# Optimization experiments

Hardware: AMD Instinct MI355X
Metric: run time of the kernel (lower is better)

## Reference

```python
import jax, jax.numpy as jnp
import numpy as np

N, IN_DIM, OUT_DIM, HEADS = 4096, 128, 32, 4
EDGE_PROB = 0.015  # ~61 neighbors/node on average


def setup_inputs() -> dict:
    key = jax.random.key(0)
    k1, k2, k3, k4 = jax.random.split(key, 4)
    x = jax.random.normal(k1, (N, IN_DIM), dtype=jnp.float32)
    adj = (jax.random.uniform(k2, (N, N)) < EDGE_PROB).astype(jnp.float32)
    adj = jnp.maximum(adj, jnp.eye(N, dtype=jnp.float32))  # self loops so softmax is never all-masked
    # nn.Linear(in_dim, out_dim*heads, bias=False): weight stored here as [in, out]
    W = jax.random.normal(k3, (IN_DIM, OUT_DIM * HEADS), dtype=jnp.float32) / np.sqrt(IN_DIM).astype(np.float32)
    # nn.Linear(2*out_dim, 1, bias=False) -> a single [2*out_dim] vector shared across heads
    a = jax.random.normal(k4, (2 * OUT_DIM,), dtype=jnp.float32) / np.sqrt(2 * OUT_DIM).astype(np.float32)
    return {"x": x, "adj": adj, "W": W, "a": a}


def reference(x, adj, W, a):
    n = x.shape[0]
    xp = (x @ W).reshape(n, HEADS, OUT_DIM)  # [N, H, D]
    # Original builds concat([x_expanded, x_j_expanded])[i,j] = [x[j] || x[i]] and applies
    # a linear map. Since attn is linear, scores decompose: e[i,j,h] = a1.x[j,h] + a2.x[i,h].
    a_j, a_i = a[:OUT_DIM], a[OUT_DIM:]
    s_j = jnp.einsum('nhd,d->nh', xp, a_j)  # contribution of column node j
    s_i = jnp.einsum('nhd,d->nh', xp, a_i)  # contribution of row node i
    scale = jnp.float32(1.0 / np.sqrt(OUT_DIM))
    e = (s_i[:, None, :] + s_j[None, :, :]) * scale  # [N, N, H]
    e = e + ((1.0 - adj) * jnp.float32(-1e9))[:, :, None]
    att = jax.nn.softmax(e, axis=1)  # softmax over dim=1 (neighbors j), as in original
    out = jnp.einsum('ijh,jhd->ihd', att, xp)  # attention-weighted neighbor aggregation
    return out.reshape(n, HEADS * OUT_DIM)
```

## Files before the change

### kernel.cpp

```cpp
#include <hip/hip_runtime.h>

#define N_NODES 4096
#define IN_DIM  128
#define OUT_DIM 32
#define HEADS   4
#define FDIM    128
#define K1_ROWS 8
#define CAP     192

static __device__ __forceinline__ unsigned bf16pack(float a, float b) {
    unsigned ua = __float_as_uint(a), ub = __float_as_uint(b);
    ua = (ua + 0x7FFFu + ((ua >> 16) & 1u)) >> 16;
    ub = (ub + 0x7FFFu + ((ub >> 16) & 1u)) >> 16;
    return ua | (ub << 16);
}

__global__ __launch_bounds__(256) void gat_proj(const float* __restrict__ x,
                                                const float* __restrict__ W,
                                                const float* __restrict__ a,
                                                unsigned* __restrict__ Ybf,
                                                float* __restrict__ Eg) {
    __shared__ float xs[K1_ROWS * IN_DIM];
    __shared__ float eS[K1_ROWS][HEADS];
    const int t    = threadIdx.x;
    const int row0 = blockIdx.x * K1_ROWS;

    ((float4*)xs)[t] = ((const float4*)(x + (size_t)row0 * IN_DIM))[t];
    __syncthreads();

    const int c  = t & 127;
    const int rg = t >> 7;
    const float* xb = xs + (rg * 4) * IN_DIM;

    float acc0 = 0.f, acc1 = 0.f, acc2 = 0.f, acc3 = 0.f;
#pragma unroll 4
    for (int k0 = 0; k0 < IN_DIM; k0 += 4) {
        const float w0 = W[(k0 + 0) * FDIM + c];
        const float w1 = W[(k0 + 1) * FDIM + c];
        const float w2 = W[(k0 + 2) * FDIM + c];
        const float w3 = W[(k0 + 3) * FDIM + c];
        const float4 x0 = *(const float4*)(xb + 0 * IN_DIM + k0);
        const float4 x1 = *(const float4*)(xb + 1 * IN_DIM + k0);
        const float4 x2 = *(const float4*)(xb + 2 * IN_DIM + k0);
        const float4 x3 = *(const float4*)(xb + 3 * IN_DIM + k0);
        acc0 = fmaf(x0.x, w0, fmaf(x0.y, w1, fmaf(x0.z, w2, fmaf(x0.w, w3, acc0))));
        acc1 = fmaf(x1.x, w0, fmaf(x1.y, w1, fmaf(x1.z, w2, fmaf(x1.w, w3, acc1))));
        acc2 = fmaf(x2.x, w0, fmaf(x2.y, w1, fmaf(x2.z, w2, fmaf(x2.w, w3, acc2))));
        acc3 = fmaf(x3.x, w0, fmaf(x3.y, w1, fmaf(x3.z, w2, fmaf(x3.w, w3, acc3))));
    }

    const int rb = rg * 4;
    __syncthreads();
    xs[(rb + 0) * FDIM + c] = acc0;
    xs[(rb + 1) * FDIM + c] = acc1;
    xs[(rb + 2) * FDIM + c] = acc2;
    xs[(rb + 3) * FDIM + c] = acc3;
    __syncthreads();

    if (t < K1_ROWS * HEADS) {
        const int r = t >> 2, h = t & 3;
        const float4* xr = (const float4*)(xs + r * FDIM + h * OUT_DIM);
        const float4* aj = (const float4*)a;
        float vj = 0.f;
#pragma unroll
        for (int q = 0; q < 8; ++q) {
            const float4 xv = xr[q], a0 = aj[q];
            vj += xv.x * a0.x + xv.y * a0.y + xv.z * a0.z + xv.w * a0.w;
        }
        const float e = __expf(vj * 0.17677669529663687f);
        eS[r][h] = e;
        Eg[(row0 + r) * HEADS + h] = e;
    }
    __syncthreads();

#pragma unroll
    for (int q = 0; q < 2; ++q) {
        const int idx = t + 256 * q;
        const int r   = idx >> 6;
        const int cp  = idx & 63;
        const float e = eS[r][cp >> 4];
        const float a0 = xs[r * FDIM + 2 * cp]     * e;
        const float a1 = xs[r * FDIM + 2 * cp + 1] * e;
        Ybf[(size_t)(row0 + r) * 64 + cp] = bf16pack(a0, a1);
    }
}

__global__ __launch_bounds__(256, 8) void gat_sum(const float* __restrict__ adj,
                                                  const unsigned* __restrict__ Ybf,
                                                  const float* __restrict__ E,
                                                  float* __restrict__ out) {
    const int tid  = threadIdx.x;
    const int wv   = tid >> 6;
    const int lane = tid & 63;
    const int row  = blockIdx.x * 2 + (wv >> 1);
    const int half = wv & 1;
    const int ll   = lane & 31;
    const int sel  = lane >> 5;
    const int hm8  = ll >> 3;

    __shared__ int    seg_s[4][CAP];
    __shared__ float4 partv[4][32];
    __shared__ float  partz[4][32];

    const float4* arow = (const float4*)(adj + (size_t)row * N_NODES) + half * 512;
    float4 v[8];
#pragma unroll
    for (int c = 0; c < 8; ++c) v[c] = arow[c * 64 + lane];

    const unsigned long long lt = (1ULL << lane) - 1ULL;
    int* seg = seg_s[wv];
    int base = 0;
#pragma unroll
    for (int c = 0; c < 8; ++c) {
        const int cb = half * 2048 + c * 256 + lane * 4;
        const float vals[4] = {v[c].x, v[c].y, v[c].z, v[c].w};
#pragma unroll
        for (int m = 0; m < 4; ++m) {
            const unsigned long long mk = __ballot(vals[m] != 0.f);
            const int pos = base + __popcll(mk & lt);
            if (vals[m] != 0.f && pos < CAP) seg[pos] = cb + m;
            base += __popcll(mk);
        }
    }
    const int cnt = base;

    const uint2* Y2 = (const uint2*)Ybf;
    float a0 = 0.f, a1 = 0.f, a2 = 0.f, a3 = 0.f, za = 0.f;
    float b0 = 0.f, b1 = 0.f, b2 = 0.f, b3 = 0.f, zb = 0.f;

#define ACCA(u, ev)                                                           \
    {                                                                         \
        a0 += __uint_as_float((u).x << 16);                                   \
        a1 += __uint_as_float((u).x & 0xFFFF0000u);                           \
        a2 += __uint_as_float((u).y << 16);                                   \
        a3 += __uint_as_float((u).y & 0xFFFF0000u);                           \
        za += (ev);                                                           \
    }
#define ACCB(u, ev)                                                           \
    {                                                                         \
        b0 += __uint_as_float((u).x << 16);                                   \
        b1 += __uint_as_float((u).x & 0xFFFF0000u);                           \
        b2 += __uint_as_float((u).y << 16);                                   \
        b3 += __uint_as_float((u).y & 0xFFFF0000u);                           \
        zb += (ev);                                                           \
    }

    if (__builtin_expect(cnt <= CAP, 1)) {
        const int npair = cnt >> 1;
        int p = 0;
        for (; p + 4 <= npair; p += 4) {
            const int4 q0 = *(const int4*)&seg[2 * p];
            const int4 q1 = *(const int4*)&seg[2 * p + 4];
            const int j0 = sel ? q0.y : q0.x;
            const int j1 = sel ? q0.w : q0.z;
            const int j2 = sel ? q1.y : q1.x;
            const int j3 = sel ? q1.w : q1.z;
            const uint2 y0 = Y2[(size_t)j0 * 32 + ll];
            const uint2 y1 = Y2[(size_t)j1 * 32 + ll];
            const uint2 y2 = Y2[(size_t)j2 * 32 + ll];
            const uint2 y3 = Y2[(size_t)j3 * 32 + ll];
            const float e0 = E[(size_t)j0 * 4 + hm8];
            const float e1 = E[(size_t)j1 * 4 + hm8];
            const float e2 = E[(size_t)j2 * 4 + hm8];
            const float e3 = E[(size_t)j3 * 4 + hm8];
            ACCA(y0, e0) ACCB(y1, e1) ACCA(y2, e2) ACCB(y3, e3)
        }
        for (; p < npair; ++p) {
            const int2 q = *(const int2*)&seg[2 * p];
            const int j = sel ? q.y : q.x;
            const uint2 y = Y2[(size_t)j * 32 + ll];
            const float e = E[(size_t)j * 4 + hm8];
            ACCA(y, e)
        }
        if (cnt & 1) {
            const int j = seg[cnt - 1];
            if (sel == 0) {
                const uint2 y = Y2[(size_t)j * 32 + ll];
                const float e = E[(size_t)j * 4 + hm8];
                ACCA(y, e)
            }
        }
    } else {
        int ep = 0;
#pragma unroll
        for (int c = 0; c < 8; ++c) {
            const float vals[4] = {v[c].x, v[c].y, v[c].z, v[c].w};
#pragma unroll
            for (int m = 0; m < 4; ++m) {
                unsigned long long mask = __ballot(vals[m] != 0.f);
                while (mask) {
                    const int b = __builtin_ctzll(mask);
                    mask &= mask - 1ULL;
                    if ((ep & 1) == sel) {
                        const int j = half * 2048 + c * 256 + b * 4 + m;
                        const uint2 y = Y2[(size_t)j * 32 + ll];
                        const float e = E[(size_t)j * 4 + hm8];
                        ACCA(y, e)
                    }
                    ++ep;
                }
            }
        }
    }
#undef ACCA
#undef ACCB

    a0 += b0; a1 += b1; a2 += b2; a3 += b3; za += zb;
    a0 += __shfl_down(a0, 32);
    a1 += __shfl_down(a1, 32);
    a2 += __shfl_down(a2, 32);
    a3 += __shfl_down(a3, 32);
    za += __shfl_down(za, 32);

    if (lane < 32) {
        partv[wv][ll] = make_float4(a0, a1, a2, a3);
        partz[wv][ll] = za;
    }
    __syncthreads();

    if ((wv & 1) == 0 && lane < 32) {
        const float4 pa = partv[wv][ll];
        const float4 pb = partv[wv + 1][ll];
        const float invZ = 1.0f / (partz[wv][ll] + partz[wv + 1][ll]);
        float4 o;
        o.x = (pa.x + pb.x) * invZ;
        o.y = (pa.y + pb.y) * invZ;
        o.z = (pa.z + pb.z) * invZ;
        o.w = (pa.w + pb.w) * invZ;
        ((float4*)out)[(size_t)row * 32 + ll] = o;
    }
}

extern "C" void kernel_launch(void* const* d_in, const int* in_sizes, int n_in,
                              void* d_out, int out_size, void* d_ws, size_t ws_size,
                              hipStream_t stream) {
    const float* x   = (const float*)d_in[0];
    const float* adj = (const float*)d_in[1];
    const float* W   = (const float*)d_in[2];
    const float* a   = (const float*)d_in[3];
    float* out = (float*)d_out;

    unsigned* Ybf = (unsigned*)d_ws;
    float*    E   = (float*)(Ybf + (size_t)N_NODES * 64);

    gat_proj<<<N_NODES / K1_ROWS, 256, 0, stream>>>(x, W, a, Ybf, E);
    gat_sum<<<N_NODES / 2, 256, 0, stream>>>(adj, Ybf, E, out);
}
```

Measured before the change: 28.27 us.

## Process two rows per block with all four waves per row and prefetch next adjacency row

gat_sum now launches half as many blocks, and each block handles two rows spaced 2048 apart. All four waves split one row into quarters, and the partial sums are reduced across the four waves through shared memory. While the current row's neighbor gather runs, the next row's adjacency slice is loaded into registers, which is meant to hide the latency of the 64 MB adjacency stream behind the gather work. Per-wave capacity drops to 128 and the unroll drops to two pairs. Costs include an extra barrier per row and fewer blocks in flight.

```diff
diff --git a/kernel.cpp b/kernel.cpp
--- a/kernel.cpp
+++ b/kernel.cpp
@@ -6,7 +6,9 @@
 #define HEADS   4
 #define FDIM    128
 #define K1_ROWS 8
-#define CAP     192
+#define CAP     128
+#define NITER   2
+#define RSTRIDE 2048
 
 static __device__ __forceinline__ unsigned bf16pack(float a, float b) {
     unsigned ua = __float_as_uint(a), ub = __float_as_uint(b);
@@ -92,8 +94,6 @@
     const int tid  = threadIdx.x;
     const int wv   = tid >> 6;
     const int lane = tid & 63;
-    const int row  = blockIdx.x * 2 + (wv >> 1);
-    const int half = wv & 1;
     const int ll   = lane & 31;
     const int sel  = lane >> 5;
     const int hm8  = ll >> 3;
@@ -102,31 +102,38 @@
     __shared__ float4 partv[4][32];
     __shared__ float  partz[4][32];
 
-    const float4* arow = (const float4*)(adj + (size_t)row * N_NODES) + half * 512;
-    float4 v[8];
-#pragma unroll
-    for (int c = 0; c < 8; ++c) v[c] = arow[c * 64 + lane];
-
     const unsigned long long lt = (1ULL << lane) - 1ULL;
     int* seg = seg_s[wv];
-    int base = 0;
-#pragma unroll
-    for (int c = 0; c < 8; ++c) {
-        const int cb = half * 2048 + c * 256 + lane * 4;
-        const float vals[4] = {v[c].x, v[c].y, v[c].z, v[c].w};
-#pragma unroll
-        for (int m = 0; m < 4; ++m) {
-            const unsigned long long mk = __ballot(vals[m] != 0.f);
-            const int pos = base + __popcll(mk & lt);
-            if (vals[m] != 0.f && pos < CAP) seg[pos] = cb + m;
-            base += __popcll(mk);
-        }
-    }
-    const int cnt = base;
-
     const uint2* Y2 = (const uint2*)Ybf;
-    float a0 = 0.f, a1 = 0.f, a2 = 0.f, a3 = 0.f, za = 0.f;
-    float b0 = 0.f, b1 = 0.f, b2 = 0.f, b3 = 0.f, zb = 0.f;
+
+    float4 v[4];
+    {
+        const float4* aq = (const float4*)(adj + (size_t)blockIdx.x * N_NODES) + wv * 256;
+#pragma unroll
+        for (int c = 0; c < 4; ++c) v[c] = aq[c * 64 + lane];
+    }
+
+#pragma unroll
+    for (int t = 0; t < NITER; ++t) {
+        const int row = blockIdx.x + RSTRIDE * t;
+
+        int base = 0;
+#pragma unroll
+        for (int c = 0; c < 4; ++c) {
+            const int cb = wv * 1024 + c * 256 + lane * 4;
+            const float vals[4] = {v[c].x, v[c].y, v[c].z, v[c].w};
+#pragma unroll
+            for (int m = 0; m < 4; ++m) {
+                const unsigned long long mk = __ballot(vals[m] != 0.f);
+                const int pos = base + __popcll(mk & lt);
+                if (vals[m] != 0.f && pos < CAP) seg[pos] = cb + m;
+                base += __popcll(mk);
+            }
+        }
+        const int cnt = base;
+
+        float a0 = 0.f, a1 = 0.f, a2 = 0.f, a3 = 0.f, za = 0.f;
+        float b0 = 0.f, b1 = 0.f, b2 = 0.f, b3 = 0.f, zb = 0.f;
 
 #define ACCA(u, ev)                                                           \
     {                                                                         \
@@ -145,89 +152,97 @@
         zb += (ev);                                                           \
     }
 
-    if (__builtin_expect(cnt <= CAP, 1)) {
-        const int npair = cnt >> 1;
-        int p = 0;
-        for (; p + 4 <= npair; p += 4) {
-            const int4 q0 = *(const int4*)&seg[2 * p];
-            const int4 q1 = *(const int4*)&seg[2 * p + 4];
-            const int j0 = sel ? q0.y : q0.x;
-            const int j1 = sel ? q0.w : q0.z;
-            const int j2 = sel ? q1.y : q1.x;
-            const int j3 = sel ? q1.w : q1.z;
-            const uint2 y0 = Y2[(size_t)j0 * 32 + ll];
-            const uint2 y1 = Y2[(size_t)j1 * 32 + ll];
-            const uint2 y2 = Y2[(size_t)j2 * 32 + ll];
-            const uint2 y3 = Y2[(size_t)j3 * 32 + ll];
-            const float e0 = E[(size_t)j0 * 4 + hm8];
-            const float e1 = E[(size_t)j1 * 4 + hm8];
-            const float e2 = E[(size_t)j2 * 4 + hm8];
-            const float e3 = E[(size_t)j3 * 4 + hm8];
-            ACCA(y0, e0) ACCB(y1, e1) ACCA(y2, e2) ACCB(y3, e3)
-        }
-        for (; p < npair; ++p) {
-            const int2 q = *(const int2*)&seg[2 * p];
-            const int j = sel ? q.y : q.x;
-            const uint2 y = Y2[(size_t)j * 32 + ll];
-            const float e = E[(size_t)j * 4 + hm8];
-            ACCA(y, e)
-        }
-        if (cnt & 1) {
-            const int j = seg[cnt - 1];
-            if (sel == 0) {
+        if (__builtin_expect(cnt <= CAP, 1)) {
+            if (t + 1 < NITER) {
+                const float4* aq =
+                    (const float4*)(adj + (size_t)(row + RSTRIDE) * N_NODES) + wv * 256;
+#pragma unroll
+                for (int c = 0; c < 4; ++c) v[c] = aq[c * 64 + lane];
+            }
+            const int npair = cnt >> 1;
+            int p = 0;
+            for (; p + 2 <= npair; p += 2) {
+                const int4 q = *(const int4*)&seg[2 * p];
+                const int j0 = sel ? q.y : q.x;
+                const int j1 = sel ? q.w : q.z;
+                const uint2 y0 = Y2[(size_t)j0 * 32 + ll];
+                const uint2 y1 = Y2[(size_t)j1 * 32 + ll];
+                const float e0 = E[(size_t)j0 * 4 + hm8];
+                const float e1 = E[(size_t)j1 * 4 + hm8];
+                ACCA(y0, e0) ACCB(y1, e1)
+            }
+            if (p < npair) {
+                const int2 q = *(const int2*)&seg[2 * p];
+                const int j = sel ? q.y : q.x;
                 const uint2 y = Y2[(size_t)j * 32 + ll];
                 const float e = E[(size_t)j * 4 + hm8];
                 ACCA(y, e)
             }
-        }
-    } else {
-        int ep = 0;
-#pragma unroll
-        for (int c = 0; c < 8; ++c) {
-            const float vals[4] = {v[c].x, v[c].y, v[c].z, v[c].w};
-#pragma unroll
-            for (int m = 0; m < 4; ++m) {
-                unsigned long long mask = __ballot(vals[m] != 0.f);
-                while (mask) {
-                    const int b = __builtin_ctzll(mask);
-                    mask &= mask - 1ULL;
-                    if ((ep & 1) == sel) {
-                        const int j = half * 2048 + c * 256 + b * 4 + m;
-                        const uint2 y = Y2[(size_t)j * 32 + ll];
-                        const float e = E[(size_t)j * 4 + hm8];
-                        ACCA(y, e)
+            if (cnt & 1) {
+                const int j = seg[cnt - 1];
+                if (sel == 0) {
+                    const uint2 y = Y2[(size_t)j * 32 + ll];
+                    const float e = E[(size_t)j * 4 + hm8];
+                    ACCA(y, e)
+                }
+            }
+        } else {
+            int ep = 0;
+#pragma unroll
+            for (int c = 0; c < 4; ++c) {
+                const float vals[4] = {v[c].x, v[c].y, v[c].z, v[c].w};
+#pragma unroll
+                for (int m = 0; m < 4; ++m) {
+                    unsigned long long mask = __ballot(vals[m] != 0.f);
+                    while (mask) {
+                        const int b = __builtin_ctzll(mask);
+                        mask &= mask - 1ULL;
+                        if ((ep & 1) == sel) {
+                            const int j = wv * 1024 + c * 256 + b * 4 + m;
+                            const uint2 y = Y2[(size_t)j * 32 + ll];
+                            const float e = E[(size_t)j * 4 + hm8];
+                            ACCA(y, e)
+                        }
+                        ++ep;
                     }
-                    ++ep;
                 }
             }
-        }
-    }
+            if (t + 1 < NITER) {
+                const float4* aq =
+                    (const float4*)(adj + (size_t)(row + RSTRIDE) * N_NODES) + wv * 256;
+#pragma unroll
+                for (int c = 0; c < 4; ++c) v[c] = aq[c * 64 + lane];
+            }
+        }
 #undef ACCA
 #undef ACCB
 
-    a0 += b0; a1 += b1; a2 += b2; a3 += b3; za += zb;
-    a0 += __shfl_down(a0, 32);
-    a1 += __shfl_down(a1, 32);
-    a2 += __shfl_down(a2, 32);
-    a3 += __shfl_down(a3, 32);
-    za += __shfl_down(za, 32);
-
-    if (lane < 32) {
-        partv[wv][ll] = make_float4(a0, a1, a2, a3);
-        partz[wv][ll] = za;
-    }
-    __syncthreads();
-
-    if ((wv & 1) == 0 && lane < 32) {
-        const float4 pa = partv[wv][ll];
-        const float4 pb = partv[wv + 1][ll];
-        const float invZ = 1.0f / (partz[wv][ll] + partz[wv + 1][ll]);
-        float4 o;
-        o.x = (pa.x + pb.x) * invZ;
-        o.y = (pa.y + pb.y) * invZ;
-        o.z = (pa.z + pb.z) * invZ;
-        o.w = (pa.w + pb.w) * invZ;
-        ((float4*)out)[(size_t)row * 32 + ll] = o;
+        a0 += b0; a1 += b1; a2 += b2; a3 += b3; za += zb;
+        a0 += __shfl_down(a0, 32);
+        a1 += __shfl_down(a1, 32);
+        a2 += __shfl_down(a2, 32);
+        a3 += __shfl_down(a3, 32);
+        za += __shfl_down(za, 32);
+        if (lane < 32) {
+            partv[wv][ll] = make_float4(a0, a1, a2, a3);
+            partz[wv][ll] = za;
+        }
+        __syncthreads();
+
+        if (wv == 0 && lane < 32) {
+            const float4 p0 = partv[0][ll], p1 = partv[1][ll];
+            const float4 p2 = partv[2][ll], p3 = partv[3][ll];
+            const float z = (partz[0][ll] + partz[1][ll]) +
+                            (partz[2][ll] + partz[3][ll]);
+            const float invZ = 1.0f / z;
+            float4 o;
+            o.x = ((p0.x + p1.x) + (p2.x + p3.x)) * invZ;
+            o.y = ((p0.y + p1.y) + (p2.y + p3.y)) * invZ;
+            o.z = ((p0.z + p1.z) + (p2.z + p3.z)) * invZ;
+            o.w = ((p0.w + p1.w) + (p2.w + p3.w)) * invZ;
+            ((float4*)out)[(size_t)row * 32 + ll] = o;
+        }
+        if (t + 1 < NITER) __syncthreads();
     }
 }
 
@@ -244,5 +259,5 @@
     float*    E   = (float*)(Ybf + (size_t)N_NODES * 64);
 
     gat_proj<<<N_NODES / K1_ROWS, 256, 0, stream>>>(x, W, a, Ybf, E);
-    gat_sum<<<N_NODES / 2, 256, 0, stream>>>(adj, Ybf, E, out);
-}
+    gat_sum<<<RSTRIDE, 256, 0, stream>>>(adj, Ybf, E, out);
+}
```

After: 29.90 us. +5.8%, slower.

## Widen gather to 16-byte loads with four neighbor groups per wavefront

Applied to the files above, without the earlier changes.

Each wavefront's neighbor gather is reorganised so that 16 lanes cover one 256-byte bf16 feature row with uint4 loads, and four lane groups handle four different neighbors at once, instead of 32 lanes with uint2 loads and two neighbors at a time. The partial sums are reduced with xor shuffles across the four groups, and the final combine writes two float4 values per lane. This halves the number of load instructions per gathered row and exposes more independent neighbor loads per iteration, which targets the gather latency. In exchange it needs more accumulator registers, uses masked tail handling and a padded segment buffer, and issues more redundant E loads per lane.

```diff
diff --git a/kernel.cpp b/kernel.cpp
--- a/kernel.cpp
+++ b/kernel.cpp
@@ -94,13 +94,12 @@
     const int lane = tid & 63;
     const int row  = blockIdx.x * 2 + (wv >> 1);
     const int half = wv & 1;
-    const int ll   = lane & 31;
-    const int sel  = lane >> 5;
-    const int hm8  = ll >> 3;
-
-    __shared__ int    seg_s[4][CAP];
-    __shared__ float4 partv[4][32];
-    __shared__ float  partz[4][32];
+    const int g    = lane >> 4;
+    const int q    = lane & 15;
+    const int head = q >> 2;
+
+    __shared__ int   seg_s[4][CAP + 16];
+    __shared__ float part[4][16][12];
 
     const float4* arow = (const float4*)(adj + (size_t)row * N_NODES) + half * 512;
     float4 v[8];
@@ -124,61 +123,56 @@
     }
     const int cnt = base;
 
-    const uint2* Y2 = (const uint2*)Ybf;
-    float a0 = 0.f, a1 = 0.f, a2 = 0.f, a3 = 0.f, za = 0.f;
-    float b0 = 0.f, b1 = 0.f, b2 = 0.f, b3 = 0.f, zb = 0.f;
-
-#define ACCA(u, ev)                                                           \
+    const uint4* Yv = (const uint4*)Ybf;
+    float a0 = 0.f, a1 = 0.f, a2 = 0.f, a3 = 0.f;
+    float a4 = 0.f, a5 = 0.f, a6 = 0.f, a7 = 0.f, z = 0.f;
+
+#define ACC(u, ev)                                                            \
     {                                                                         \
         a0 += __uint_as_float((u).x << 16);                                   \
         a1 += __uint_as_float((u).x & 0xFFFF0000u);                           \
         a2 += __uint_as_float((u).y << 16);                                   \
         a3 += __uint_as_float((u).y & 0xFFFF0000u);                           \
-        za += (ev);                                                           \
-    }
-#define ACCB(u, ev)                                                           \
-    {                                                                         \
-        b0 += __uint_as_float((u).x << 16);                                   \
-        b1 += __uint_as_float((u).x & 0xFFFF0000u);                           \
-        b2 += __uint_as_float((u).y << 16);                                   \
-        b3 += __uint_as_float((u).y & 0xFFFF0000u);                           \
-        zb += (ev);                                                           \
+        a4 += __uint_as_float((u).z << 16);                                   \
+        a5 += __uint_as_float((u).z & 0xFFFF0000u);                           \
+        a6 += __uint_as_float((u).w << 16);                                   \
+        a7 += __uint_as_float((u).w & 0xFFFF0000u);                           \
+        z  += (ev);                                                           \
     }
 
     if (__builtin_expect(cnt <= CAP, 1)) {
-        const int npair = cnt >> 1;
         int p = 0;
-        for (; p + 4 <= npair; p += 4) {
-            const int4 q0 = *(const int4*)&seg[2 * p];
-            const int4 q1 = *(const int4*)&seg[2 * p + 4];
-            const int j0 = sel ? q0.y : q0.x;
-            const int j1 = sel ? q0.w : q0.z;
-            const int j2 = sel ? q1.y : q1.x;
-            const int j3 = sel ? q1.w : q1.z;
-            const uint2 y0 = Y2[(size_t)j0 * 32 + ll];
-            const uint2 y1 = Y2[(size_t)j1 * 32 + ll];
-            const uint2 y2 = Y2[(size_t)j2 * 32 + ll];
-            const uint2 y3 = Y2[(size_t)j3 * 32 + ll];
-            const float e0 = E[(size_t)j0 * 4 + hm8];
-            const float e1 = E[(size_t)j1 * 4 + hm8];
-            const float e2 = E[(size_t)j2 * 4 + hm8];
-            const float e3 = E[(size_t)j3 * 4 + hm8];
-            ACCA(y0, e0) ACCB(y1, e1) ACCA(y2, e2) ACCB(y3, e3)
-        }
-        for (; p < npair; ++p) {
-            const int2 q = *(const int2*)&seg[2 * p];
-            const int j = sel ? q.y : q.x;
-            const uint2 y = Y2[(size_t)j * 32 + ll];
-            const float e = E[(size_t)j * 4 + hm8];
-            ACCA(y, e)
-        }
-        if (cnt & 1) {
-            const int j = seg[cnt - 1];
-            if (sel == 0) {
-                const uint2 y = Y2[(size_t)j * 32 + ll];
-                const float e = E[(size_t)j * 4 + hm8];
-                ACCA(y, e)
-            }
+        for (; p + 16 <= cnt; p += 16) {
+            const int4 jq = *(const int4*)&seg[p + 4 * g];
+            const uint4 y0 = Yv[(size_t)jq.x * 16 + q];
+            const uint4 y1 = Yv[(size_t)jq.y * 16 + q];
+            const uint4 y2 = Yv[(size_t)jq.z * 16 + q];
+            const uint4 y3 = Yv[(size_t)jq.w * 16 + q];
+            const float e0 = E[(size_t)jq.x * 4 + head];
+            const float e1 = E[(size_t)jq.y * 4 + head];
+            const float e2 = E[(size_t)jq.z * 4 + head];
+            const float e3 = E[(size_t)jq.w * 4 + head];
+            ACC(y0, e0) ACC(y1, e1) ACC(y2, e2) ACC(y3, e3)
+        }
+        if (p < cnt) {
+            const int eb = p + 4 * g;
+            const int4 jq = *(const int4*)&seg[eb];
+            const bool k0 = eb + 0 < cnt, k1 = eb + 1 < cnt;
+            const bool k2 = eb + 2 < cnt, k3 = eb + 3 < cnt;
+            const int j0 = k0 ? jq.x : 0, j1 = k1 ? jq.y : 0;
+            const int j2 = k2 ? jq.z : 0, j3 = k3 ? jq.w : 0;
+            const uint4 y0 = Yv[(size_t)j0 * 16 + q];
+            const uint4 y1 = Yv[(size_t)j1 * 16 + q];
+            const uint4 y2 = Yv[(size_t)j2 * 16 + q];
+            const uint4 y3 = Yv[(size_t)j3 * 16 + q];
+            const float e0 = E[(size_t)j0 * 4 + head];
+            const float e1 = E[(size_t)j1 * 4 + head];
+            const float e2 = E[(size_t)j2 * 4 + head];
+            const float e3 = E[(size_t)j3 * 4 + head];
+            if (k0) ACC(y0, e0)
+            if (k1) ACC(y1, e1)
+            if (k2) ACC(y2, e2)
+            if (k3) ACC(y3, e3)
         }
     } else {
         int ep = 0;
@@ -191,43 +185,56 @@
                 while (mask) {
                     const int b = __builtin_ctzll(mask);
                     mask &= mask - 1ULL;
-                    if ((ep & 1) == sel) {
+                    if ((ep & 3) == g) {
                         const int j = half * 2048 + c * 256 + b * 4 + m;
-                        const uint2 y = Y2[(size_t)j * 32 + ll];
-                        const float e = E[(size_t)j * 4 + hm8];
-                        ACCA(y, e)
+                        const uint4 y = Yv[(size_t)j * 16 + q];
+                        const float e = E[(size_t)j * 4 + head];
+                        ACC(y, e)
                     }
                     ++ep;
                 }
             }
         }
     }
-#undef ACCA
-#undef ACCB
-
-    a0 += b0; a1 += b1; a2 += b2; a3 += b3; za += zb;
-    a0 += __shfl_down(a0, 32);
-    a1 += __shfl_down(a1, 32);
-    a2 += __shfl_down(a2, 32);
-    a3 += __shfl_down(a3, 32);
-    za += __shfl_down(za, 32);
-
-    if (lane < 32) {
-        partv[wv][ll] = make_float4(a0, a1, a2, a3);
-        partz[wv][ll] = za;
-    }
-    __syncthreads();
-
-    if ((wv & 1) == 0 && lane < 32) {
-        const float4 pa = partv[wv][ll];
-        const float4 pb = partv[wv + 1][ll];
-        const float invZ = 1.0f / (partz[wv][ll] + partz[wv + 1][ll]);
-        float4 o;
-        o.x = (pa.x + pb.x) * invZ;
-        o.y = (pa.y + pb.y) * invZ;
-        o.z = (pa.z + pb.z) * invZ;
-        o.w = (pa.w + pb.w) * invZ;
-        ((float4*)out)[(size_t)row * 32 + ll] = o;
+#undef ACC
+
+#pragma unroll
+    for (int off = 16; off < 64; off <<= 1) {
+        a0 += __shfl_xor(a0, off);
+        a1 += __shfl_xor(a1, off);
+        a2 += __shfl_xor(a2, off);
+        a3 += __shfl_xor(a3, off);
+        a4 += __shfl_xor(a4, off);
+        a5 += __shfl_xor(a5, off);
+        a6 += __shfl_xor(a6, off);
+        a7 += __shfl_xor(a7, off);
+        z  += __shfl_xor(z, off);
+    }
+
+    if (lane < 16) {
+        float* pr = part[wv][q];
+        pr[0] = a0; pr[1] = a1; pr[2] = a2; pr[3] = a3;
+        pr[4] = a4; pr[5] = a5; pr[6] = a6; pr[7] = a7;
+        pr[8] = z;
+    }
+    __syncthreads();
+
+    if ((wv & 1) == 0 && lane < 16) {
+        const float* pa = part[wv][q];
+        const float* pb = part[wv + 1][q];
+        const float invZ = 1.0f / (pa[8] + pb[8]);
+        float4 o0, o1;
+        o0.x = (pa[0] + pb[0]) * invZ;
+        o0.y = (pa[1] + pb[1]) * invZ;
+        o0.z = (pa[2] + pb[2]) * invZ;
+        o0.w = (pa[3] + pb[3]) * invZ;
+        o1.x = (pa[4] + pb[4]) * invZ;
+        o1.y = (pa[5] + pb[5]) * invZ;
+        o1.z = (pa[6] + pb[6]) * invZ;
+        o1.w = (pa[7] + pb[7]) * invZ;
+        float4* orow = (float4*)(out + (size_t)row * FDIM + q * 8);
+        orow[0] = o0;
+        orow[1] = o1;
     }
 }
 
```

Result: no change. 27.83 us (-1.6%).
